# Kernel tuning notes

Measured on AMD Instinct MI355X. Metric: run time of the kernel, lower is better.

## Reference

```python
import jax, jax.numpy as jnp
import numpy as np

N_NODES = 100000
N_EDGES = 1600000


def _glorot(key, shape):
    lim = float(np.sqrt(6.0 / (shape[0] + shape[1])))
    return jax.random.uniform(key, shape, jnp.float32, -lim, lim)


def setup_inputs() -> dict:
    key = jax.random.key(0)
    ks = jax.random.split(key, 12)
    x = jax.random.normal(ks[0], (N_NODES, 8), jnp.float32)
    edge_index = jax.random.randint(ks[1], (2, N_EDGES), 0, N_NODES, jnp.int64)
    dims = [(8, 32), (32, 32), (32, 32), (32, 32), (32, 3)]
    params = {}
    for i, (din, dout) in enumerate(dims):
        params[f"W{i+1}"] = _glorot(ks[2 + i], (din, dout))
        params[f"b{i+1}"] = jnp.zeros((dout,), jnp.float32)
    return {"x": x, "edge_index": edge_index, **params}


def _gcn_norm(edge_index, num_nodes):
    # add self-loops, symmetric normalization (PyG GCNConv defaults)
    loops = jnp.arange(num_nodes, dtype=edge_index.dtype)
    row = jnp.concatenate([edge_index[0], loops])
    col = jnp.concatenate([edge_index[1], loops])
    deg = jax.ops.segment_sum(jnp.ones_like(col, jnp.float32), col,
                              num_segments=num_nodes)
    dinv = jnp.where(deg > 0, jax.lax.rsqrt(deg), 0.0)
    norm = dinv[row] * dinv[col]  # [E + N]
    return row, col, norm


def _gcn_conv(h, W, b, row, col, norm, num_nodes):
    h = h @ W                                   # [N, dout]
    msg = h[row] * norm[:, None]                # gather + scale
    out = jax.ops.segment_sum(msg, col, num_segments=num_nodes)
    return out + b


def reference(x, edge_index, W1, b1, W2, b2, W3, b3, W4, b4, W5, b5):
    row, col, norm = _gcn_norm(edge_index, N_NODES)
    lrelu = lambda h: jax.nn.leaky_relu(h, negative_slope=1.0)  # identity, kept faithful
    h = lrelu(_gcn_conv(x, W1, b1, row, col, norm, N_NODES))
    h = lrelu(_gcn_conv(h, W2, b2, row, col, norm, N_NODES))
    h = lrelu(_gcn_conv(h, W3, b3, row, col, norm, N_NODES))
    h = lrelu(_gcn_conv(h, W4, b4, row, col, norm, N_NODES))
    h = lrelu(_gcn_conv(h, W5, b5, row, col, norm, N_NODES))
    return h
```

## Files before the change

kernel.cpp:

```cpp
#include <hip/hip_runtime.h>
#include <hip/hip_bf16.h>

#define NN 100000
#define NE 1600000
#define NB 391
#define EPB 4096
#define NBLK 391
#define CAP 4608



__global__ __launch_bounds__(256) void prep_kernel(
    const unsigned int* __restrict__ ew, int* __restrict__ is64,
    const float* __restrict__ W1, const float* __restrict__ b1,
    const float* __restrict__ W2, const float* __restrict__ b2,
    const float* __restrict__ W3, const float* __restrict__ b3,
    const float* __restrict__ W4, const float* __restrict__ b4,
    const float* __restrict__ W5, const float* __restrict__ b5,
    float* __restrict__ Wt, float* __restrict__ cv,
    int* __restrict__ bcursor) {
    __shared__ int nz;
    __shared__ float w45[32 * 3], w345[32 * 3], w2345[32 * 3];
    int tid = threadIdx.x;
    if (tid == 0) nz = 0;
    __syncthreads();
    if (ew[2 * tid + 1] != 0) atomicAdd(&nz, 1);
    for (int i = tid; i < NB; i += 256) bcursor[i] = i * CAP;
    int i = tid / 3, j = tid - 3 * (tid / 3);
    if (tid < 96) {
        float s = 0.0f;
        for (int k = 0; k < 32; k++) s += W4[i * 32 + k] * W5[k * 3 + j];
        w45[i * 3 + j] = s;
    }
    __syncthreads();
    if (tid < 96) {
        float s = 0.0f;
        for (int k = 0; k < 32; k++) s += W3[i * 32 + k] * w45[k * 3 + j];
        w345[i * 3 + j] = s;
    }
    __syncthreads();
    if (tid < 96) {
        float s = 0.0f;
        for (int k = 0; k < 32; k++) s += W2[i * 32 + k] * w345[k * 3 + j];
        w2345[i * 3 + j] = s;
    }
    __syncthreads();
    if (tid < 32) {
        int ii = tid >> 2, jj = tid & 3;
        float s = 0.0f;
        if (jj < 3)
            for (int k = 0; k < 32; k++) s += W1[ii * 32 + k] * w2345[k * 3 + jj];
        Wt[tid] = s;
    }
    if (tid >= 32 && tid < 52) {
        int kk = (tid - 32) >> 2, jj = (tid - 32) & 3;
        float s = 0.0f;
        if (jj < 3) {
            if (kk == 0) for (int k = 0; k < 32; k++) s += b1[k] * w2345[k * 3 + jj];
            if (kk == 1) for (int k = 0; k < 32; k++) s += b2[k] * w345[k * 3 + jj];
            if (kk == 2) for (int k = 0; k < 32; k++) s += b3[k] * w45[k * 3 + jj];
            if (kk == 3) for (int k = 0; k < 32; k++) s += b4[k] * W5[k * 3 + jj];
            if (kk == 4) s = b5[jj];
        }
        cv[tid - 32] = s;
    }
    if (tid == 0) *is64 = (nz == 0) ? 1 : 0;
}


__global__ __launch_bounds__(512) void bucket_scatter_kernel(const void* __restrict__ ei,
                                                             const int* __restrict__ is64,
                                                             int* __restrict__ bcursor,
                                                             unsigned int* __restrict__ epacked,
                                                             int E) {
    __shared__ int lcount[NB];
    __shared__ int lstart[NB];
    __shared__ int lcur[NB];
    __shared__ int gbase[NB];
    __shared__ int ps[512];
    __shared__ unsigned int slotv[EPB];
    __shared__ unsigned short slotb[EPB];
    int tid = threadIdx.x;
    for (int i = tid; i < NB; i += 512) lcount[i] = 0;
    __syncthreads();
    int f = *is64;
    int base = blockIdx.x * EPB;
    int r[8], c[8];
    if (f == 0) {
        const int* e32 = (const int*)ei;
        const int4* e4 = (const int4*)ei;
#pragma unroll
        for (int k4 = 0; k4 < 2; k4++) {
            int e = base + (k4 * 512 + tid) * 4;
            if (e + 3 < E) {
                int4 v = e4[(base >> 2) + k4 * 512 + tid];
                r[4 * k4 + 0] = v.x; r[4 * k4 + 1] = v.y;
                r[4 * k4 + 2] = v.z; r[4 * k4 + 3] = v.w;
                int4 w = e4[((E + base) >> 2) + k4 * 512 + tid];
                c[4 * k4 + 0] = w.x; c[4 * k4 + 1] = w.y;
                c[4 * k4 + 2] = w.z; c[4 * k4 + 3] = w.w;
            } else {
#pragma unroll
                for (int j = 0; j < 4; j++) {
                    if (e + j < E) {
                        r[4 * k4 + j] = e32[e + j];
                        c[4 * k4 + j] = e32[E + e + j];
                    } else {
                        r[4 * k4 + j] = -1;
                    }
                }
            }
        }
    } else {
        const long long* e64 = (const long long*)ei;
#pragma unroll
        for (int k = 0; k < 8; k++) {
            int e = base + k * 512 + tid;
            if (e < E) {
                r[k] = (int)e64[e];
                c[k] = (int)e64[(long long)E + e];
            } else {
                r[k] = -1;
            }
        }
    }
#pragma unroll
    for (int k = 0; k < 8; k++)
        if (r[k] >= 0) atomicAdd(&lcount[c[k] >> 8], 1);
    __syncthreads();
    int v = (tid < NB) ? lcount[tid] : 0;
    int acc = v;
    ps[tid] = v;
    __syncthreads();
    for (int off = 1; off < 512; off <<= 1) {
        int y = (tid >= off) ? ps[tid - off] : 0;
        __syncthreads();
        acc += y;
        ps[tid] = acc;
        __syncthreads();
    }
    if (tid < NB) {
        int excl = acc - v;
        lstart[tid] = excl;
        lcur[tid] = excl;
    }
    __syncthreads();
#pragma unroll
    for (int k = 0; k < 8; k++) {
        if (r[k] >= 0) {
            int b = c[k] >> 8;
            int pos = atomicAdd(&lcur[b], 1);
            slotv[pos] = ((unsigned)(c[k] & 255) << 24) | (unsigned)r[k];
            slotb[pos] = (unsigned short)b;
        }
    }
    __syncthreads();
    for (int i = tid; i < NB; i += 512) {
        int cnt = lcount[i];
        gbase[i] = cnt ? atomicAdd(&bcursor[i], cnt) : 0;
    }
    __syncthreads();
    int rem = E - base;
    int total = (rem < EPB) ? rem : EPB;
    for (int s2 = tid; s2 < total; s2 += 512) {
        int b = slotb[s2];
        int dst = gbase[b] + (s2 - lstart[b]);
        if (dst < (b + 1) * CAP) epacked[dst] = slotv[s2];
    }
}


__global__ __launch_bounds__(512) void bucket_csr_kernel(const unsigned int* __restrict__ epacked,
                                                         const int* __restrict__ bcursor,
                                                         const float* __restrict__ x,
                                                         const float* __restrict__ Wt,
                                                         int* __restrict__ start,
                                                         int* __restrict__ degi,
                                                         float* __restrict__ dinv,
                                                         int* __restrict__ srow,
                                                         float4* __restrict__ Ta, int N) {
    __shared__ int lcount[256];
    __shared__ int lcur[256];
    __shared__ int ss[256];
    __shared__ float4 Wl[8];
    int b = blockIdx.x;
    int tid = threadIdx.x;
    if (tid < 8) Wl[tid] = ((const float4*)Wt)[tid];
    int s0 = b * CAP;
    int cnt = bcursor[b] - s0;
    if (cnt > CAP) cnt = CAP;
    if (tid < 256) lcount[tid] = 0;
    __syncthreads();
    for (int i = tid; i < cnt; i += 512) {
        unsigned int v = epacked[s0 + i];
        atomicAdd(&lcount[v >> 24], 1);
    }
    __syncthreads();
    int myc = 0, acc = 0;
    if (tid < 256) {
        myc = lcount[tid];
        acc = myc;
        ss[tid] = myc;
    }
    __syncthreads();
    for (int off = 1; off < 256; off <<= 1) {
        int y = 0;
        if (tid < 256 && tid >= off) y = ss[tid - off];
        __syncthreads();
        if (tid < 256) {
            acc += y;
            ss[tid] = acc;
        }
        __syncthreads();
    }
    if (tid < 256) {
        int excl = acc - myc;
        lcur[tid] = excl;
        int col = (b << 8) + tid;
        if (col < N) {
            start[col] = s0 + excl;
            degi[col] = myc;
            float d = 1.0f / sqrtf((float)myc + 1.0f);
            dinv[col] = d;
            const float4* x4 = (const float4*)x + col * 2;
            float4 av = x4[0], bv = x4[1];
            float xs[8] = {av.x, av.y, av.z, av.w, bv.x, bv.y, bv.z, bv.w};
            float4 o = make_float4(0.f, 0.f, 0.f, 0.f);
#pragma unroll
            for (int k = 0; k < 8; k++) {
                float4 w = Wl[k];
                o.x += xs[k] * w.x; o.y += xs[k] * w.y; o.z += xs[k] * w.z;
            }
            o.x *= d; o.y *= d; o.z *= d; o.w = 0.0f;
            Ta[col] = o;
        }
    }
    __syncthreads();
    for (int i = tid; i < cnt; i += 512) {
        unsigned int v = epacked[s0 + i];
        int p = atomicAdd(&lcur[v >> 24], 1);
        srow[s0 + p] = (int)(v & 0xFFFFFFu);
    }
}


template <bool LAST>
__global__ __launch_bounds__(256) void prop_kernel(
    const int* __restrict__ start, const int* __restrict__ degi,
    const int* __restrict__ srow, const float4* __restrict__ tin,
    const float* __restrict__ dinv, const float* __restrict__ cv, int k,
    float4* __restrict__ tout, float* __restrict__ out, int N) {
    int tid = blockIdx.x * 256 + threadIdx.x;
    int c = tid >> 3, q = tid & 7;
    if (c >= N) return;
    int s = start[c];
    int d = degi[c];
    float4 a = (q == 0) ? tin[c] : make_float4(0.f, 0.f, 0.f, 0.f);
    float4 a2 = make_float4(0.f, 0.f, 0.f, 0.f);
    int i = q;
    for (; i + 8 < d; i += 16) {
        int r0 = srow[s + i];
        int r1 = srow[s + i + 8];
        float4 v0 = tin[r0];
        float4 v1 = tin[r1];
        a.x += v0.x; a.y += v0.y; a.z += v0.z;
        a2.x += v1.x; a2.y += v1.y; a2.z += v1.z;
    }
    if (i < d) {
        float4 v = tin[srow[s + i]];
        a.x += v.x; a.y += v.y; a.z += v.z;
    }
    a.x += a2.x; a.y += a2.y; a.z += a2.z;
    a.x += __shfl_xor(a.x, 1); a.y += __shfl_xor(a.y, 1); a.z += __shfl_xor(a.z, 1);
    a.x += __shfl_xor(a.x, 2); a.y += __shfl_xor(a.y, 2); a.z += __shfl_xor(a.z, 2);
    a.x += __shfl_xor(a.x, 4); a.y += __shfl_xor(a.y, 4); a.z += __shfl_xor(a.z, 4);
    if (q == 0) {
        float dd = dinv[c];
        float cx = cv[k * 4 + 0], cy = cv[k * 4 + 1], cz = cv[k * 4 + 2];
        if (LAST) {
            out[c * 3 + 0] = dd * a.x + cx;
            out[c * 3 + 1] = dd * a.y + cy;
            out[c * 3 + 2] = dd * a.z + cz;
        } else {
            float d2 = dd * dd;
            float4 o;
            o.x = d2 * a.x + dd * cx;
            o.y = d2 * a.y + dd * cy;
            o.z = d2 * a.z + dd * cz;
            o.w = 0.0f;
            tout[c] = o;
        }
    }
}


extern "C" void kernel_launch(void* const* d_in, const int* in_sizes, int n_in,
                              void* d_out, int out_size, void* d_ws, size_t ws_size,
                              hipStream_t stream) {
    const float* x  = (const float*)d_in[0];
    const void*  ei = d_in[1];
    const float* W1 = (const float*)d_in[2];  const float* b1 = (const float*)d_in[3];
    const float* W2 = (const float*)d_in[4];  const float* b2 = (const float*)d_in[5];
    const float* W3 = (const float*)d_in[6];  const float* b3 = (const float*)d_in[7];
    const float* W4 = (const float*)d_in[8];  const float* b4 = (const float*)d_in[9];
    const float* W5 = (const float*)d_in[10]; const float* b5 = (const float*)d_in[11];
    float* out = (float*)d_out;

    char* p = (char*)d_ws;
    auto alloc = [&](size_t bytes) {
        char* r = p;
        p += (bytes + 255) & ~(size_t)255;
        return r;
    };
    int*   degi    = (int*)alloc(NN * 4);
    float* dinv    = (float*)alloc(NN * 4);
    int*   start   = (int*)alloc(NN * 4);
    int*   is64    = (int*)alloc(256);
    int*   bcursor = (int*)alloc(NB * 4);
    float* Wt      = (float*)alloc(8 * 4 * 4);
    float* cv      = (float*)alloc(5 * 4 * 4);
    unsigned int* epacked = (unsigned int*)alloc((size_t)NB * CAP * 4);
    int*          srow    = (int*)alloc((size_t)NB * CAP * 4);
    float4*       Ta      = (float4*)alloc((size_t)NN * 16);
    float4*       Tb      = (float4*)alloc((size_t)NN * 16);
    if ((size_t)(p - (char*)d_ws) > ws_size) return;

    int gP = (NN * 8 + 255) / 256;
    prep_kernel<<<1, 256, 0, stream>>>((const unsigned int*)ei, is64,
                                       W1, b1, W2, b2, W3, b3, W4, b4, W5, b5,
                                       Wt, cv, bcursor);
    bucket_scatter_kernel<<<NBLK, 512, 0, stream>>>(ei, is64, bcursor, epacked, NE);
    bucket_csr_kernel<<<NB, 512, 0, stream>>>(epacked, bcursor, x, Wt,
                                              start, degi, dinv, srow, Ta, NN);

    prop_kernel<false><<<gP, 256, 0, stream>>>(start, degi, srow, Ta, dinv, cv, 0, Tb, nullptr, NN);
    prop_kernel<false><<<gP, 256, 0, stream>>>(start, degi, srow, Tb, dinv, cv, 1, Ta, nullptr, NN);
    prop_kernel<false><<<gP, 256, 0, stream>>>(start, degi, srow, Ta, dinv, cv, 2, Tb, nullptr, NN);
    prop_kernel<false><<<gP, 256, 0, stream>>>(start, degi, srow, Tb, dinv, cv, 3, Ta, nullptr, NN);
    prop_kernel<true><<<gP, 256, 0, stream>>>(start, degi, srow, Ta, dinv, cv, 4, nullptr, out, NN);
}
```

Baseline: 175.1 us.

## Replace global-atomic bucket scatter with per-block count matrix and gather-based CSR build

Removes the single-block prep kernel by folding the dtype detection into the scatter kernel and the weight-chain products into the CSR kernel, which every block recomputes. The scatter kernel now writes each block's locally sorted edges contiguously, plus per-bucket counts and offsets, instead of using global atomic cursors into fixed-capacity buckets. The CSR kernel, using twice as many finer buckets of 128 columns, gathers its segments from every scatter block via a prefix scan into shared memory before building the column-sorted row list. This saves one launch and the global atomics, at the cost of serial per-thread gather loops, redundant weight math in each block, and silent truncation when a bucket exceeds its capacity.

Result: no change. 175.2 us (+0.0%).

```diff
diff --git a/kernel.cpp b/kernel.cpp
--- a/kernel.cpp
+++ b/kernel.cpp
@@ -3,87 +3,31 @@
 
 #define NN 100000
 #define NE 1600000
-#define NB 391
+#define NBK 782
 #define EPB 4096
 #define NBLK 391
-#define CAP 4608
-
-
-
-__global__ __launch_bounds__(256) void prep_kernel(
-    const unsigned int* __restrict__ ew, int* __restrict__ is64,
-    const float* __restrict__ W1, const float* __restrict__ b1,
-    const float* __restrict__ W2, const float* __restrict__ b2,
-    const float* __restrict__ W3, const float* __restrict__ b3,
-    const float* __restrict__ W4, const float* __restrict__ b4,
-    const float* __restrict__ W5, const float* __restrict__ b5,
-    float* __restrict__ Wt, float* __restrict__ cv,
-    int* __restrict__ bcursor) {
+#define CAPS 2560
+#define LBUF 2560
+
+
+
+__global__ __launch_bounds__(512) void scatter_kernel(const void* __restrict__ ei,
+                                                      unsigned int* __restrict__ epacked,
+                                                      int* __restrict__ gcnt,
+                                                      int* __restrict__ lofs, int E) {
     __shared__ int nz;
-    __shared__ float w45[32 * 3], w345[32 * 3], w2345[32 * 3];
+    __shared__ int lcount[NBK];
+    __shared__ int lstart[NBK];
+    __shared__ int lcur[NBK];
+    __shared__ int ps[512];
+    __shared__ unsigned int slotv[EPB];
     int tid = threadIdx.x;
     if (tid == 0) nz = 0;
-    __syncthreads();
-    if (ew[2 * tid + 1] != 0) atomicAdd(&nz, 1);
-    for (int i = tid; i < NB; i += 256) bcursor[i] = i * CAP;
-    int i = tid / 3, j = tid - 3 * (tid / 3);
-    if (tid < 96) {
-        float s = 0.0f;
-        for (int k = 0; k < 32; k++) s += W4[i * 32 + k] * W5[k * 3 + j];
-        w45[i * 3 + j] = s;
-    }
-    __syncthreads();
-    if (tid < 96) {
-        float s = 0.0f;
-        for (int k = 0; k < 32; k++) s += W3[i * 32 + k] * w45[k * 3 + j];
-        w345[i * 3 + j] = s;
-    }
-    __syncthreads();
-    if (tid < 96) {
-        float s = 0.0f;
-        for (int k = 0; k < 32; k++) s += W2[i * 32 + k] * w345[k * 3 + j];
-        w2345[i * 3 + j] = s;
-    }
-    __syncthreads();
-    if (tid < 32) {
-        int ii = tid >> 2, jj = tid & 3;
-        float s = 0.0f;
-        if (jj < 3)
-            for (int k = 0; k < 32; k++) s += W1[ii * 32 + k] * w2345[k * 3 + jj];
-        Wt[tid] = s;
-    }
-    if (tid >= 32 && tid < 52) {
-        int kk = (tid - 32) >> 2, jj = (tid - 32) & 3;
-        float s = 0.0f;
-        if (jj < 3) {
-            if (kk == 0) for (int k = 0; k < 32; k++) s += b1[k] * w2345[k * 3 + jj];
-            if (kk == 1) for (int k = 0; k < 32; k++) s += b2[k] * w345[k * 3 + jj];
-            if (kk == 2) for (int k = 0; k < 32; k++) s += b3[k] * w45[k * 3 + jj];
-            if (kk == 3) for (int k = 0; k < 32; k++) s += b4[k] * W5[k * 3 + jj];
-            if (kk == 4) s = b5[jj];
-        }
-        cv[tid - 32] = s;
-    }
-    if (tid == 0) *is64 = (nz == 0) ? 1 : 0;
-}
-
-
-__global__ __launch_bounds__(512) void bucket_scatter_kernel(const void* __restrict__ ei,
-                                                             const int* __restrict__ is64,
-                                                             int* __restrict__ bcursor,
-                                                             unsigned int* __restrict__ epacked,
-                                                             int E) {
-    __shared__ int lcount[NB];
-    __shared__ int lstart[NB];
-    __shared__ int lcur[NB];
-    __shared__ int gbase[NB];
-    __shared__ int ps[512];
-    __shared__ unsigned int slotv[EPB];
-    __shared__ unsigned short slotb[EPB];
-    int tid = threadIdx.x;
-    for (int i = tid; i < NB; i += 512) lcount[i] = 0;
-    __syncthreads();
-    int f = *is64;
+    for (int i = tid; i < NBK; i += 512) lcount[i] = 0;
+    __syncthreads();
+    if (tid < 256 && ((const unsigned int*)ei)[2 * tid + 1] != 0) atomicAdd(&nz, 1);
+    __syncthreads();
+    int f = (nz == 0) ? 1 : 0;
     int base = blockIdx.x * EPB;
     int r[8], c[8];
     if (f == 0) {
@@ -126,11 +70,12 @@
     }
 #pragma unroll
     for (int k = 0; k < 8; k++)
-        if (r[k] >= 0) atomicAdd(&lcount[c[k] >> 8], 1);
-    __syncthreads();
-    int v = (tid < NB) ? lcount[tid] : 0;
-    int acc = v;
-    ps[tid] = v;
+        if (r[k] >= 0) atomicAdd(&lcount[c[k] >> 7], 1);
+    __syncthreads();
+    int e0 = (2 * tid < NBK) ? lcount[2 * tid] : 0;
+    int e1 = (2 * tid + 1 < NBK) ? lcount[2 * tid + 1] : 0;
+    int sum = e0 + e1, acc = sum;
+    ps[tid] = sum;
     __syncthreads();
     for (int off = 1; off < 512; off <<= 1) {
         int y = (tid >= off) ? ps[tid - off] : 0;
@@ -139,86 +84,138 @@
         ps[tid] = acc;
         __syncthreads();
     }
-    if (tid < NB) {
-        int excl = acc - v;
-        lstart[tid] = excl;
-        lcur[tid] = excl;
-    }
+    int excl = acc - sum;
+    if (2 * tid < NBK) { lstart[2 * tid] = excl; lcur[2 * tid] = excl; }
+    if (2 * tid + 1 < NBK) { lstart[2 * tid + 1] = excl + e0; lcur[2 * tid + 1] = excl + e0; }
     __syncthreads();
 #pragma unroll
     for (int k = 0; k < 8; k++) {
         if (r[k] >= 0) {
-            int b = c[k] >> 8;
+            int b = c[k] >> 7;
             int pos = atomicAdd(&lcur[b], 1);
-            slotv[pos] = ((unsigned)(c[k] & 255) << 24) | (unsigned)r[k];
-            slotb[pos] = (unsigned short)b;
-        }
-    }
-    __syncthreads();
-    for (int i = tid; i < NB; i += 512) {
-        int cnt = lcount[i];
-        gbase[i] = cnt ? atomicAdd(&bcursor[i], cnt) : 0;
+            slotv[pos] = ((unsigned)(c[k] & 127) << 24) | (unsigned)r[k];
+        }
     }
     __syncthreads();
     int rem = E - base;
     int total = (rem < EPB) ? rem : EPB;
-    for (int s2 = tid; s2 < total; s2 += 512) {
-        int b = slotb[s2];
-        int dst = gbase[b] + (s2 - lstart[b]);
-        if (dst < (b + 1) * CAP) epacked[dst] = slotv[s2];
+    for (int i = tid; i < total; i += 512) epacked[base + i] = slotv[i];
+    for (int b = tid; b < NBK; b += 512) {
+        gcnt[blockIdx.x * NBK + b] = lcount[b];
+        lofs[blockIdx.x * NBK + b] = lstart[b];
     }
 }
 
 
-__global__ __launch_bounds__(512) void bucket_csr_kernel(const unsigned int* __restrict__ epacked,
-                                                         const int* __restrict__ bcursor,
-                                                         const float* __restrict__ x,
-                                                         const float* __restrict__ Wt,
-                                                         int* __restrict__ start,
-                                                         int* __restrict__ degi,
-                                                         float* __restrict__ dinv,
-                                                         int* __restrict__ srow,
-                                                         float4* __restrict__ Ta, int N) {
-    __shared__ int lcount[256];
-    __shared__ int lcur[256];
-    __shared__ int ss[256];
-    __shared__ float4 Wl[8];
+__global__ __launch_bounds__(256) void csr_kernel(
+    const unsigned int* __restrict__ epacked, const int* __restrict__ gcnt,
+    const int* __restrict__ lofs, const float* __restrict__ x,
+    const float* __restrict__ W1, const float* __restrict__ b1,
+    const float* __restrict__ W2, const float* __restrict__ b2,
+    const float* __restrict__ W3, const float* __restrict__ b3,
+    const float* __restrict__ W4, const float* __restrict__ b4,
+    const float* __restrict__ W5, const float* __restrict__ b5,
+    int* __restrict__ start, int* __restrict__ degi, float* __restrict__ dinv,
+    int* __restrict__ srow, float4* __restrict__ Ta, float* __restrict__ cv, int N) {
+    __shared__ float w45[96], w345[96], w2345[96], Wts[32];
+    __shared__ int ps[256];
+    __shared__ int hc[128], hs[128], hcur[128];
+    __shared__ unsigned int lbuf[LBUF];
+    __shared__ int stot;
     int b = blockIdx.x;
     int tid = threadIdx.x;
-    if (tid < 8) Wl[tid] = ((const float4*)Wt)[tid];
-    int s0 = b * CAP;
-    int cnt = bcursor[b] - s0;
-    if (cnt > CAP) cnt = CAP;
-    if (tid < 256) lcount[tid] = 0;
-    __syncthreads();
-    for (int i = tid; i < cnt; i += 512) {
-        unsigned int v = epacked[s0 + i];
-        atomicAdd(&lcount[v >> 24], 1);
-    }
-    __syncthreads();
-    int myc = 0, acc = 0;
-    if (tid < 256) {
-        myc = lcount[tid];
-        acc = myc;
-        ss[tid] = myc;
-    }
+
+    int wi = tid / 3, wj = tid - 3 * (tid / 3);
+    if (tid < 96) {
+        float s = 0.0f;
+        for (int k = 0; k < 32; k++) s += W4[wi * 32 + k] * W5[k * 3 + wj];
+        w45[tid] = s;
+    }
+    __syncthreads();
+    if (tid < 96) {
+        float s = 0.0f;
+        for (int k = 0; k < 32; k++) s += W3[wi * 32 + k] * w45[k * 3 + wj];
+        w345[tid] = s;
+    }
+    __syncthreads();
+    if (tid < 96) {
+        float s = 0.0f;
+        for (int k = 0; k < 32; k++) s += W2[wi * 32 + k] * w345[k * 3 + wj];
+        w2345[tid] = s;
+    }
+    __syncthreads();
+    if (tid < 32) {
+        int ii = tid >> 2, jj = tid & 3;
+        float s = 0.0f;
+        if (jj < 3)
+            for (int k = 0; k < 32; k++) s += W1[ii * 32 + k] * w2345[k * 3 + jj];
+        Wts[tid] = s;
+    }
+    if (b == 0 && tid >= 32 && tid < 52) {
+        int kk = (tid - 32) >> 2, jj = (tid - 32) & 3;
+        float s = 0.0f;
+        if (jj < 3) {
+            if (kk == 0) for (int k = 0; k < 32; k++) s += b1[k] * w2345[k * 3 + jj];
+            if (kk == 1) for (int k = 0; k < 32; k++) s += b2[k] * w345[k * 3 + jj];
+            if (kk == 2) for (int k = 0; k < 32; k++) s += b3[k] * w45[k * 3 + jj];
+            if (kk == 3) for (int k = 0; k < 32; k++) s += b4[k] * W5[k * 3 + jj];
+            if (kk == 4) s = b5[jj];
+        }
+        cv[tid - 32] = s;
+    }
+
+    int k0 = 2 * tid, k1 = 2 * tid + 1;
+    int c0 = (k0 < NBLK) ? gcnt[k0 * NBK + b] : 0;
+    int c1 = (k1 < NBLK) ? gcnt[k1 * NBK + b] : 0;
+    int sum = c0 + c1, acc = sum;
+    ps[tid] = sum;
     __syncthreads();
     for (int off = 1; off < 256; off <<= 1) {
+        int y = (tid >= off) ? ps[tid - off] : 0;
+        __syncthreads();
+        acc += y;
+        ps[tid] = acc;
+        __syncthreads();
+    }
+    int excl = acc - sum;
+    if (tid == 255) stot = acc;
+    __syncthreads();
+    int total = stot;
+    if (total > LBUF) total = LBUF;
+    if (c0 > 0) {
+        int src = k0 * EPB + lofs[k0 * NBK + b];
+        for (int i = 0; i < c0; i++) {
+            int d = excl + i;
+            if (d < LBUF) lbuf[d] = epacked[src + i];
+        }
+    }
+    if (c1 > 0) {
+        int src = k1 * EPB + lofs[k1 * NBK + b];
+        for (int i = 0; i < c1; i++) {
+            int d = excl + c0 + i;
+            if (d < LBUF) lbuf[d] = epacked[src + i];
+        }
+    }
+    if (tid < 128) hc[tid] = 0;
+    __syncthreads();
+    for (int i = tid; i < total; i += 256) atomicAdd(&hc[lbuf[i] >> 24], 1);
+    __syncthreads();
+    int myc = 0, a2 = 0;
+    if (tid < 128) { myc = hc[tid]; a2 = myc; hs[tid] = myc; }
+    __syncthreads();
+    for (int off = 1; off < 128; off <<= 1) {
         int y = 0;
-        if (tid < 256 && tid >= off) y = ss[tid - off];
-        __syncthreads();
-        if (tid < 256) {
-            acc += y;
-            ss[tid] = acc;
-        }
-        __syncthreads();
-    }
-    if (tid < 256) {
-        int excl = acc - myc;
-        lcur[tid] = excl;
-        int col = (b << 8) + tid;
+        if (tid < 128 && tid >= off) y = hs[tid - off];
+        __syncthreads();
+        if (tid < 128) { a2 += y; hs[tid] = a2; }
+        __syncthreads();
+    }
+    if (tid < 128) {
+        int ex = a2 - myc;
+        hcur[tid] = ex;
+        int col = (b << 7) + tid;
         if (col < N) {
-            start[col] = s0 + excl;
+            start[col] = b * CAPS + ex;
             degi[col] = myc;
             float d = 1.0f / sqrtf((float)myc + 1.0f);
             dinv[col] = d;
@@ -228,18 +225,19 @@
             float4 o = make_float4(0.f, 0.f, 0.f, 0.f);
 #pragma unroll
             for (int k = 0; k < 8; k++) {
-                float4 w = Wl[k];
-                o.x += xs[k] * w.x; o.y += xs[k] * w.y; o.z += xs[k] * w.z;
+                o.x += xs[k] * Wts[4 * k + 0];
+                o.y += xs[k] * Wts[4 * k + 1];
+                o.z += xs[k] * Wts[4 * k + 2];
             }
             o.x *= d; o.y *= d; o.z *= d; o.w = 0.0f;
             Ta[col] = o;
         }
     }
     __syncthreads();
-    for (int i = tid; i < cnt; i += 512) {
-        unsigned int v = epacked[s0 + i];
-        int p = atomicAdd(&lcur[v >> 24], 1);
-        srow[s0 + p] = (int)(v & 0xFFFFFFu);
+    for (int i = tid; i < total; i += 256) {
+        unsigned int v = lbuf[i];
+        int p = atomicAdd(&hcur[v >> 24], 1);
+        srow[b * CAPS + p] = (int)(v & 0xFFFFFFu);
     }
 }
 
@@ -312,26 +310,23 @@
         p += (bytes + 255) & ~(size_t)255;
         return r;
     };
-    int*   degi    = (int*)alloc(NN * 4);
-    float* dinv    = (float*)alloc(NN * 4);
-    int*   start   = (int*)alloc(NN * 4);
-    int*   is64    = (int*)alloc(256);
-    int*   bcursor = (int*)alloc(NB * 4);
-    float* Wt      = (float*)alloc(8 * 4 * 4);
-    float* cv      = (float*)alloc(5 * 4 * 4);
-    unsigned int* epacked = (unsigned int*)alloc((size_t)NB * CAP * 4);
-    int*          srow    = (int*)alloc((size_t)NB * CAP * 4);
+    int*   degi = (int*)alloc(NN * 4);
+    float* dinv = (float*)alloc(NN * 4);
+    int*   start = (int*)alloc(NN * 4);
+    float* cv   = (float*)alloc(5 * 4 * 4);
+    unsigned int* epacked = (unsigned int*)alloc((size_t)NBLK * EPB * 4);
+    int*          gcnt    = (int*)alloc((size_t)NBLK * NBK * 4);
+    int*          lofs    = (int*)alloc((size_t)NBLK * NBK * 4);
+    int*          srow    = (int*)alloc((size_t)NBK * CAPS * 4);
     float4*       Ta      = (float4*)alloc((size_t)NN * 16);
     float4*       Tb      = (float4*)alloc((size_t)NN * 16);
     if ((size_t)(p - (char*)d_ws) > ws_size) return;
 
     int gP = (NN * 8 + 255) / 256;
-    prep_kernel<<<1, 256, 0, stream>>>((const unsigned int*)ei, is64,
-                                       W1, b1, W2, b2, W3, b3, W4, b4, W5, b5,
-                                       Wt, cv, bcursor);
-    bucket_scatter_kernel<<<NBLK, 512, 0, stream>>>(ei, is64, bcursor, epacked, NE);
-    bucket_csr_kernel<<<NB, 512, 0, stream>>>(epacked, bcursor, x, Wt,
-                                              start, degi, dinv, srow, Ta, NN);
+    scatter_kernel<<<NBLK, 512, 0, stream>>>(ei, epacked, gcnt, lofs, NE);
+    csr_kernel<<<NBK, 256, 0, stream>>>(epacked, gcnt, lofs, x,
+                                        W1, b1, W2, b2, W3, b3, W4, b4, W5, b5,
+                                        start, degi, dinv, srow, Ta, cv, NN);
 
     prop_kernel<false><<<gP, 256, 0, stream>>>(start, degi, srow, Ta, dinv, cv, 0, Tb, nullptr, NN);
     prop_kernel<false><<<gP, 256, 0, stream>>>(start, degi, srow, Tb, dinv, cv, 1, Ta, nullptr, NN);
```
